# Performance work log

Measured on AMD Instinct MI355X. Metric: run time of the kernel, lower is better.

The kernel has to match this reference:

```python
import jax, jax.numpy as jnp
import numpy as np

H = 2048  # hidden_size
I = 2048  # input_size
B = 2048  # batch


def setup_inputs() -> dict:
    key = jax.random.key(0)
    k0, k1, k2, k3, k4, k5 = jax.random.split(key, 6)
    # bipolar-domain activations live in [-1, 1]
    inp = jax.random.uniform(k0, (B, I), jnp.float32, minval=-1.0, maxval=1.0)
    hx = jax.random.uniform(k1, (B, H), jnp.float32, minval=-1.0, maxval=1.0)
    s = 1.0 / np.sqrt(H + I)
    w_f = jax.random.normal(k2, (H, H + I), jnp.float32) * s
    b_f = jax.random.normal(k3, (H,), jnp.float32) * s
    w_n = jax.random.normal(k4, (H, H + I), jnp.float32) * s
    b_n = jax.random.normal(k5, (H,), jnp.float32) * s
    return {"input": inp, "hx": hx, "w_f": w_f, "b_f": b_f, "w_n": w_n, "b_n": b_n}


def reference(input, hx, w_f, b_f, w_n, b_n):
    # Expected-value (probability-domain) math of the unary bitstream MGU cell.
    # fg_ug_tanh: FSULinear on [hx, x]; 'hardtanh is direct pass' -> identity act.
    fg_ug_in = jnp.concatenate([hx, input], axis=1)            # [B, H+I]
    fg_in = fg_ug_in @ w_f.T + b_f                              # [B, H]
    # fg_sigmoid: FSUAdd of [fg_in, ones] with scale=None -> (x + 1) / 2
    fg = (fg_in + 1.0) * 0.5                                    # [B, H]
    # fg_hx_mul: FSUMul with static in_1_prob = hx buffer
    fg_hx = fg * hx                                             # [B, H]
    # ng_ug_tanh: FSULinear on [fg*hx, x]
    ng_ug_in = jnp.concatenate([fg_hx, input], axis=1)          # [B, H+I]
    ng = ng_ug_in @ w_n.T + b_n                                 # [B, H]
    # fg_ng_mul: dynamic FSUMul; bipolar bit-inversion (1 - bitstream) negates value
    fg_ng = fg * ng
    # hy_add: FSUAdd([ng, -fg*ng, fg*hx], scale=1) -> plain sum
    hy = ng - fg_ng + fg_hx                                     # = (1-fg)*ng + fg*hx
    return hy
```

## Files before the change

kernel.cpp:

```cpp
#include <hip/hip_runtime.h>
#include <stdint.h>


#define Hdim 2048
#define Idim 2048
#define Bdim 2048
#define Ktot 4096
#define KHALF 2048
#define NSTEP 64
#define NSTEP2 32

typedef __bf16 bf16;
typedef __bf16 bf16x8 __attribute__((ext_vector_type(8)));
typedef float  f32x4  __attribute__((ext_vector_type(4)));

__device__ __forceinline__ void gload_lds16(const bf16* g, bf16* l) {
  __builtin_amdgcn_global_load_lds(
      (const __attribute__((address_space(1))) unsigned int*)g,
      (__attribute__((address_space(3))) unsigned int*)l,
      16, 0, 0);
}

__device__ __forceinline__ void cvt8(const float* __restrict__ src, bf16* __restrict__ dst) {
  const float4* s = (const float4*)src;
  float4 a = s[0], b = s[1];
  bf16x8 o;
  o[0]=(bf16)a.x; o[1]=(bf16)a.y; o[2]=(bf16)a.z; o[3]=(bf16)a.w;
  o[4]=(bf16)b.x; o[5]=(bf16)b.y; o[6]=(bf16)b.z; o[7]=(bf16)b.w;
  *(bf16x8*)dst = o;
}

__global__ void prep_kernel(const float* __restrict__ w_f, const float* __restrict__ w_n,
                            const float* __restrict__ hx, const float* __restrict__ x,
                            bf16* __restrict__ Wf, bf16* __restrict__ Wn,
                            bf16* __restrict__ A1) {
  const int n8 = Hdim * Ktot / 8;
  int stride = gridDim.x * blockDim.x;
  for (int i = blockIdx.x * blockDim.x + threadIdx.x; i < 3 * n8; i += stride) {
    if (i < n8) {
      cvt8(w_f + (size_t)i * 8, Wf + (size_t)i * 8);
    } else if (i < 2 * n8) {
      int j = i - n8;
      cvt8(w_n + (size_t)j * 8, Wn + (size_t)j * 8);
    } else {
      int j = i - 2 * n8;
      int e = j * 8;
      int b = e >> 12;
      int k = e & (Ktot - 1);
      const float* src = (k < Hdim) ? (hx + (size_t)b * Hdim + k)
                                    : (x  + (size_t)b * Idim + (k - Hdim));
      cvt8(src, A1 + (size_t)e);
    }
  }
}

template<int EPI>
__global__ __launch_bounds__(128, 1)
void gemm_kernel(const bf16* __restrict__ Ab0, int sA0,
                 const bf16* __restrict__ Ab1, int sA1,
                 const bf16* __restrict__ W,
                 const float* __restrict__ bias,
                 const float* __restrict__ hx,
                 bf16* __restrict__ OMF,
                 bf16* __restrict__ A2L,
                 float* __restrict__ OUT)
{
  __shared__ bf16 lds[3][12288];

  int bid  = blockIdx.x;
  int sbid = (bid & 7) * 64 + (bid >> 3);
  int tm = sbid >> 5, tn = sbid & 31;

  int tid = threadIdx.x;
  int w = tid >> 6, lane = tid & 63;
  int wrow = w * 64;
  int fr = lane & 15, fq = lane >> 4;
  int swz = fr & 7;

  int srow = tid >> 3;
  int csrc = (tid & 7) ^ (srow & 7);

  const bf16* pA0 = Ab0 + (size_t)(tm * 128 + srow) * sA0 + csrc * 8;
  const bf16* pA1 = Ab1 + (size_t)(tm * 128 + srow) * sA1 + csrc * 8;
  const bf16* pB  = W   + (size_t)(tn * 64  + srow) * Ktot + csrc * 8;
  int lb = w * 512;

#define STAGE(pbuf, t_) do {                                                   \
    const bf16* pa_ = ((t_) < NSTEP2) ? pA0 : pA1;                             \
    size_t sa_ = ((t_) < NSTEP2) ? (size_t)sA0 : (size_t)sA1;                  \
    size_t ko_ = ((t_) < NSTEP2) ? (size_t)(t_) * 64 : (size_t)((t_) - NSTEP2) * 64; \
    _Pragma("unroll")                                                          \
    for (int jj = 0; jj < 8; ++jj)                                             \
      gload_lds16(pa_ + (size_t)jj * 16 * sa_ + ko_, (pbuf) + jj * 1024 + lb); \
    _Pragma("unroll")                                                          \
    for (int jj = 0; jj < 4; ++jj)                                             \
      gload_lds16(pB + (size_t)jj * 16 * Ktot + (size_t)(t_) * 64,             \
                  (pbuf) + 8192 + jj * 1024 + lb);                             \
  } while (0)

  f32x4 acc[4][4] = {};

#define COMPUTE(pbuf) do {                                                     \
    _Pragma("unroll")                                                          \
    for (int kk = 0; kk < 2; ++kk) {                                           \
      bf16x8 af[4], bv[4];                                                     \
      int ch = ((kk * 4 + fq) ^ swz) * 8;                                      \
      _Pragma("unroll")                                                        \
      for (int m = 0; m < 4; ++m)                                              \
        af[m] = *(const bf16x8*)((pbuf) + (wrow + m * 16 + fr) * 64 + ch);     \
      _Pragma("unroll")                                                        \
      for (int n = 0; n < 4; ++n)                                              \
        bv[n] = *(const bf16x8*)((pbuf) + 8192 + (n * 16 + fr) * 64 + ch);     \
      __builtin_amdgcn_s_setprio(1);                                           \
      _Pragma("unroll")                                                        \
      for (int m = 0; m < 4; ++m)                                              \
        _Pragma("unroll")                                                      \
        for (int n = 0; n < 4; ++n)                                            \
          acc[m][n] = __builtin_amdgcn_mfma_f32_16x16x32_bf16(af[m], bv[n], acc[m][n], 0, 0, 0); \
      __builtin_amdgcn_s_setprio(0);                                           \
    }                                                                          \
  } while (0)

  bf16* p0 = &lds[0][0];
  bf16* p1 = &lds[1][0];
  bf16* p2 = &lds[2][0];

  STAGE(p0, 0);
  STAGE(p1, 1);
  #pragma unroll 1
  for (int t = 0; t < NSTEP; ++t) {
    if (t < NSTEP - 1) asm volatile("s_waitcnt vmcnt(12)" ::: "memory");
    else               asm volatile("s_waitcnt vmcnt(0)" ::: "memory");
    __builtin_amdgcn_s_barrier();
    asm volatile("" ::: "memory");
    if (t + 2 < NSTEP) STAGE(p2, t + 2);
    COMPUTE(p0);
    bf16* tmp = p0; p0 = p1; p1 = p2; p2 = tmp;
  }
#undef COMPUTE
#undef STAGE

  int row0 = tm * 128 + wrow + fq * 4;
  int col0 = tn * 64 + fr;
  #pragma unroll
  for (int n = 0; n < 4; ++n) {
    int gcol = col0 + n * 16;
    float bv2 = bias[gcol];
    #pragma unroll
    for (int m = 0; m < 4; ++m) {
      #pragma unroll
      for (int i = 0; i < 4; ++i) {
        int grow = row0 + m * 16 + i;
        size_t idx = (size_t)grow * Hdim + gcol;
        float v = acc[m][n][i] + bv2;
        if (EPI == 0) {
          float fg = (v + 1.0f) * 0.5f;
          OMF[idx] = (bf16)(1.0f - fg);
          A2L[idx] = (bf16)(fg * hx[idx]);
        } else {
          OUT[idx] = (float)OMF[idx] * v + (float)A2L[idx];
        }
      }
    }
  }
}

extern "C" void kernel_launch(void* const* d_in, const int* in_sizes, int n_in,
                              void* d_out, int out_size, void* d_ws, size_t ws_size,
                              hipStream_t stream) {
  const float* x   = (const float*)d_in[0];
  const float* hx  = (const float*)d_in[1];
  const float* w_f = (const float*)d_in[2];
  const float* b_f = (const float*)d_in[3];
  const float* w_n = (const float*)d_in[4];
  const float* b_n = (const float*)d_in[5];
  float* out = (float*)d_out;

  bf16* A1  = (bf16*)d_ws;
  bf16* A2L = A1  + (size_t)Bdim * Ktot;
  bf16* Wf  = A2L + (size_t)Bdim * KHALF;
  bf16* Wn  = Wf  + (size_t)Hdim * Ktot;
  bf16* OMF = Wn  + (size_t)Hdim * Ktot;

  prep_kernel<<<2048, 256, 0, stream>>>(w_f, w_n, hx, x, Wf, Wn, A1);

  gemm_kernel<0><<<512, 128, 0, stream>>>(A1, Ktot, A1 + KHALF, Ktot, Wf, b_f,
                                          hx, OMF, A2L, nullptr);
  gemm_kernel<1><<<512, 128, 0, stream>>>(A2L, KHALF, A1 + Hdim, Ktot, Wn, b_n,
                                          nullptr, OMF, A2L, out);
}
```

Measured before the change: 133.0 us.

## Split K across two wave groups per block with LDS reduction

Doubles the block to 256 threads and assigns each pair of waves half of the K dimension, each with its own triple-buffered LDS ring at a 32-wide K step. Partial accumulators from the second group are exchanged through LDS and summed before the fused epilogue. The aim is more waves in flight and more latency hiding per output tile, at the cost of more barriers per unit of work, a final reduction, and more LDS per block.

```diff
diff --git a/kernel.cpp b/kernel.cpp
--- a/kernel.cpp
+++ b/kernel.cpp
@@ -8,7 +8,6 @@
 #define Ktot 4096
 #define KHALF 2048
 #define NSTEP 64
-#define NSTEP2 32
 
 typedef __bf16 bf16;
 typedef __bf16 bf16x8 __attribute__((ext_vector_type(8)));
@@ -55,7 +54,7 @@
 }
 
 template<int EPI>
-__global__ __launch_bounds__(128, 1)
+__global__ __launch_bounds__(256, 2)
 void gemm_kernel(const bf16* __restrict__ Ab0, int sA0,
                  const bf16* __restrict__ Ab1, int sA1,
                  const bf16* __restrict__ W,
@@ -65,7 +64,7 @@
                  bf16* __restrict__ A2L,
                  float* __restrict__ OUT)
 {
-  __shared__ bf16 lds[3][12288];
+  __shared__ bf16 lds[2][3][6144];
 
   int bid  = blockIdx.x;
   int sbid = (bid & 7) * 64 + (bid >> 3);
@@ -73,63 +72,69 @@
 
   int tid = threadIdx.x;
   int w = tid >> 6, lane = tid & 63;
-  int wrow = w * 64;
+  int g = w >> 1, wg = w & 1;
+  int wrow = wg * 64;
   int fr = lane & 15, fq = lane >> 4;
-  int swz = fr & 7;
-
-  int srow = tid >> 3;
-  int csrc = (tid & 7) ^ (srow & 7);
-
-  const bf16* pA0 = Ab0 + (size_t)(tm * 128 + srow) * sA0 + csrc * 8;
-  const bf16* pA1 = Ab1 + (size_t)(tm * 128 + srow) * sA1 + csrc * 8;
-  const bf16* pB  = W   + (size_t)(tn * 64  + srow) * Ktot + csrc * 8;
-  int lb = w * 512;
+  int ch = (fq ^ (fr & 3)) * 8;
+
+  int gtid = wg * 64 + lane;
+  int srow = gtid >> 2;
+  int csrc = (gtid & 3) ^ (srow & 3);
+
+  const bf16* pA;
+  size_t strA;
+  if (EPI == 0) {
+    pA = (g == 0) ? Ab0 : Ab1;
+    strA = (g == 0) ? (size_t)sA0 : (size_t)sA1;
+    pA += (size_t)(tm * 128 + srow) * strA + csrc * 8 + g * KHALF;
+  } else if (g == 0) {
+    pA = Ab0 + (size_t)(tm * 128 + srow) * sA0 + csrc * 8;
+    strA = sA0;
+  } else {
+    pA = Ab1 + (size_t)(tm * 128 + srow) * sA1 + csrc * 8;
+    strA = sA1;
+  }
+  const bf16* pB = W + (size_t)(tn * 64 + srow) * Ktot + csrc * 8 + g * KHALF;
+  int lb = wg * 512;
 
 #define STAGE(pbuf, t_) do {                                                   \
-    const bf16* pa_ = ((t_) < NSTEP2) ? pA0 : pA1;                             \
-    size_t sa_ = ((t_) < NSTEP2) ? (size_t)sA0 : (size_t)sA1;                  \
-    size_t ko_ = ((t_) < NSTEP2) ? (size_t)(t_) * 64 : (size_t)((t_) - NSTEP2) * 64; \
-    _Pragma("unroll")                                                          \
-    for (int jj = 0; jj < 8; ++jj)                                             \
-      gload_lds16(pa_ + (size_t)jj * 16 * sa_ + ko_, (pbuf) + jj * 1024 + lb); \
+    size_t ko_ = (size_t)(t_) * 32;                                            \
     _Pragma("unroll")                                                          \
     for (int jj = 0; jj < 4; ++jj)                                             \
-      gload_lds16(pB + (size_t)jj * 16 * Ktot + (size_t)(t_) * 64,             \
-                  (pbuf) + 8192 + jj * 1024 + lb);                             \
+      gload_lds16(pA + (size_t)jj * 32 * strA + ko_, (pbuf) + jj * 1024 + lb); \
+    _Pragma("unroll")                                                          \
+    for (int jj = 0; jj < 2; ++jj)                                             \
+      gload_lds16(pB + (size_t)jj * 32 * Ktot + ko_, (pbuf) + 4096 + jj * 1024 + lb); \
   } while (0)
 
   f32x4 acc[4][4] = {};
 
 #define COMPUTE(pbuf) do {                                                     \
-    _Pragma("unroll")                                                          \
-    for (int kk = 0; kk < 2; ++kk) {                                           \
-      bf16x8 af[4], bv[4];                                                     \
-      int ch = ((kk * 4 + fq) ^ swz) * 8;                                      \
-      _Pragma("unroll")                                                        \
-      for (int m = 0; m < 4; ++m)                                              \
-        af[m] = *(const bf16x8*)((pbuf) + (wrow + m * 16 + fr) * 64 + ch);     \
+    bf16x8 af[4], bv[4];                                                       \
+    _Pragma("unroll")                                                          \
+    for (int m = 0; m < 4; ++m)                                                \
+      af[m] = *(const bf16x8*)((pbuf) + (wrow + m * 16 + fr) * 32 + ch);       \
+    _Pragma("unroll")                                                          \
+    for (int n = 0; n < 4; ++n)                                                \
+      bv[n] = *(const bf16x8*)((pbuf) + 4096 + (n * 16 + fr) * 32 + ch);       \
+    __builtin_amdgcn_s_setprio(1);                                             \
+    _Pragma("unroll")                                                          \
+    for (int m = 0; m < 4; ++m)                                                \
       _Pragma("unroll")                                                        \
       for (int n = 0; n < 4; ++n)                                              \
-        bv[n] = *(const bf16x8*)((pbuf) + 8192 + (n * 16 + fr) * 64 + ch);     \
-      __builtin_amdgcn_s_setprio(1);                                           \
-      _Pragma("unroll")                                                        \
-      for (int m = 0; m < 4; ++m)                                              \
-        _Pragma("unroll")                                                      \
-        for (int n = 0; n < 4; ++n)                                            \
-          acc[m][n] = __builtin_amdgcn_mfma_f32_16x16x32_bf16(af[m], bv[n], acc[m][n], 0, 0, 0); \
-      __builtin_amdgcn_s_setprio(0);                                           \
-    }                                                                          \
+        acc[m][n] = __builtin_amdgcn_mfma_f32_16x16x32_bf16(af[m], bv[n], acc[m][n], 0, 0, 0); \
+    __builtin_amdgcn_s_setprio(0);                                             \
   } while (0)
 
-  bf16* p0 = &lds[0][0];
-  bf16* p1 = &lds[1][0];
-  bf16* p2 = &lds[2][0];
+  bf16* p0 = &lds[g][0][0];
+  bf16* p1 = &lds[g][1][0];
+  bf16* p2 = &lds[g][2][0];
 
   STAGE(p0, 0);
   STAGE(p1, 1);
   #pragma unroll 1
   for (int t = 0; t < NSTEP; ++t) {
-    if (t < NSTEP - 1) asm volatile("s_waitcnt vmcnt(12)" ::: "memory");
+    if (t < NSTEP - 1) asm volatile("s_waitcnt vmcnt(6)" ::: "memory");
     else               asm volatile("s_waitcnt vmcnt(0)" ::: "memory");
     __builtin_amdgcn_s_barrier();
     asm volatile("" ::: "memory");
@@ -140,25 +145,38 @@
 #undef COMPUTE
 #undef STAGE
 
-  int row0 = tm * 128 + wrow + fq * 4;
-  int col0 = tn * 64 + fr;
-  #pragma unroll
-  for (int n = 0; n < 4; ++n) {
-    int gcol = col0 + n * 16;
-    float bv2 = bias[gcol];
+  __syncthreads();
+  float* xch = (float*)&lds[0][0][0];
+  if (g == 1) {
     #pragma unroll
-    for (int m = 0; m < 4; ++m) {
+    for (int m = 0; m < 4; ++m)
       #pragma unroll
-      for (int i = 0; i < 4; ++i) {
-        int grow = row0 + m * 16 + i;
-        size_t idx = (size_t)grow * Hdim + gcol;
-        float v = acc[m][n][i] + bv2;
-        if (EPI == 0) {
-          float fg = (v + 1.0f) * 0.5f;
-          OMF[idx] = (bf16)(1.0f - fg);
-          A2L[idx] = (bf16)(fg * hx[idx]);
-        } else {
-          OUT[idx] = (float)OMF[idx] * v + (float)A2L[idx];
+      for (int n = 0; n < 4; ++n)
+        *(f32x4*)&xch[wg * 4096 + (m * 4 + n) * 256 + lane * 4] = acc[m][n];
+  }
+  __syncthreads();
+  if (g == 0) {
+    int row0 = tm * 128 + wrow + fq * 4;
+    int col0 = tn * 64 + fr;
+    #pragma unroll
+    for (int n = 0; n < 4; ++n) {
+      int gcol = col0 + n * 16;
+      float bv2 = bias[gcol];
+      #pragma unroll
+      for (int m = 0; m < 4; ++m) {
+        f32x4 part = *(const f32x4*)&xch[wg * 4096 + (m * 4 + n) * 256 + lane * 4];
+        #pragma unroll
+        for (int i = 0; i < 4; ++i) {
+          int grow = row0 + m * 16 + i;
+          size_t idx = (size_t)grow * Hdim + gcol;
+          float v = acc[m][n][i] + part[i] + bv2;
+          if (EPI == 0) {
+            float fg = (v + 1.0f) * 0.5f;
+            OMF[idx] = (bf16)(1.0f - fg);
+            A2L[idx] = (bf16)(fg * hx[idx]);
+          } else {
+            OUT[idx] = (float)OMF[idx] * v + (float)A2L[idx];
+          }
         }
       }
     }
@@ -184,8 +202,8 @@
 
   prep_kernel<<<2048, 256, 0, stream>>>(w_f, w_n, hx, x, Wf, Wn, A1);
 
-  gemm_kernel<0><<<512, 128, 0, stream>>>(A1, Ktot, A1 + KHALF, Ktot, Wf, b_f,
+  gemm_kernel<0><<<512, 256, 0, stream>>>(A1, Ktot, A1, Ktot, Wf, b_f,
                                           hx, OMF, A2L, nullptr);
-  gemm_kernel<1><<<512, 128, 0, stream>>>(A2L, KHALF, A1 + Hdim, Ktot, Wn, b_n,
+  gemm_kernel<1><<<512, 256, 0, stream>>>(A2L, KHALF, A1 + Hdim, Ktot, Wn, b_n,
                                           nullptr, OMF, A2L, out);
 }
```

Measured after the change: 149.0 us. +12.0%, slower.
